# Performance work log

Measured on AMD Instinct MI355X. Metric: run time of the kernel, lower is better.

Reference implementation:

```python
import jax, jax.numpy as jnp
import numpy as np

B, S, D, H = 1, 2048, 768, 12
E, K, I = 8, 2, 1024          # routed experts, top-k, expert inter dim
IS = 2 * I                    # shared-expert inter dim (n_shared_experts * moe_inter_dim)
EPS = 1e-5
ROUTE_SCALE = 1.0


def rmsnorm(x, w, eps=EPS):
    xf = x.astype(jnp.float32)
    return (xf * jax.lax.rsqrt(jnp.mean(xf * xf, axis=-1, keepdims=True) + eps)).astype(x.dtype) * w


def setup_inputs() -> dict:
    key = jax.random.key(0)
    ks = jax.random.split(key, 8)
    sc = 0.02
    return {
        "x": jax.random.normal(ks[0], (B, S, D), jnp.float32),
        "norm1_w": jnp.ones((D,), jnp.float32),
        "norm3_w": jnp.ones((D,), jnp.float32),
        "gate_w": jax.random.normal(ks[1], (E, D), jnp.float32) * sc,
        "w1": jax.random.normal(ks[2], (E, I, D), jnp.float32) * sc,
        "b1": jnp.zeros((E, I), jnp.float32),
        "w2": jax.random.normal(ks[3], (E, D, I), jnp.float32) * sc,
        "b2": jnp.zeros((E, D), jnp.float32),
        "w3": jax.random.normal(ks[4], (E, I, D), jnp.float32) * sc,
        "b3": jnp.zeros((E, I), jnp.float32),
        "fc1_w": jax.random.normal(ks[5], (IS, D), jnp.float32) * sc,
        "fc1_b": jnp.zeros((IS,), jnp.float32),
        "fc2_w": jax.random.normal(ks[6], (D, IS), jnp.float32) * sc,
        "fc2_b": jnp.zeros((D,), jnp.float32),
    }


def _forward(x, norm1_w, norm3_w, gate_w, w1, b1, w2, b2, w3, b3,
             fc1_w, fc1_b, fc2_w, fc2_b):
    b, s, d = x.shape
    hd = d // H

    # ---- self-attention (no qkv/out projections in the original module) ----
    xn = rmsnorm(x, norm1_w)
    qkv = xn.reshape(b, s, H, hd).transpose(0, 2, 1, 3)      # [b,h,s,hd]
    scores = jnp.einsum("bhqd,bhkd->bhqk", qkv, qkv) / np.sqrt(hd)
    attn = jax.nn.softmax(scores, axis=-1)
    ao = jnp.einsum("bhqk,bhkd->bhqd", attn, qkv)
    attn_out = ao.transpose(0, 2, 1, 3).reshape(b, s, d)
    out = x + attn_out

    # ---- MoE on norm3(out) ----
    xf = rmsnorm(out, norm3_w).reshape(-1, d)                # [N, D]
    n = xf.shape[0]

    # Gate: softmax scoring, n_groups=1 (no group masking), no bias (dim != 7168)
    logits = xf @ gate_w.T                                    # [N, E]
    sc = jax.nn.softmax(logits.astype(jnp.float32), axis=-1)  # max-subtract folded in
    _, idx = jax.lax.top_k(sc, K)                             # [N, K]
    weights = jnp.take_along_axis(sc, idx, axis=-1)
    weights = jnp.clip(weights, 1e-7) * ROUTE_SCALE
    weights = weights.astype(xf.dtype)

    # combine matrix: per-token dense expert weights (zeros for unselected)
    cmb = jnp.zeros((n, E), xf.dtype).at[jnp.arange(n)[:, None], idx].add(weights)

    # SwiGLU experts, batched over E (zero combine weight == not dispatched)
    a = jnp.einsum("nd,eid->nei", xf, w1) + b1                # [N,E,I]
    g = jnp.einsum("nd,eid->nei", xf, w3) + b3
    h = jax.nn.silu(a) * g
    eo = jnp.einsum("nei,edi->ned", h, w2) + b2               # [N,E,D]
    y = jnp.einsum("ned,ne->nd", eo, cmb)

    # shared experts (SiLU MLP)
    z = jax.nn.silu(xf @ fc1_w.T + fc1_b) @ fc2_w.T + fc2_b

    moe_out = (y + z).reshape(b, s, d)
    return out + moe_out


def reference(x, norm1_w, norm3_w, gate_w, w1, b1, w2, b2, w3, b3,
              fc1_w, fc1_b, fc2_w, fc2_b):
    return _forward(x, norm1_w, norm3_w, gate_w, w1, b1, w2, b2, w3, b3,
                    fc1_w, fc1_b, fc2_w, fc2_b)
```

## Files before the change

kernel.cpp:

```cpp
#include <hip/hip_runtime.h>
#include <math.h>

#define SEQ    2048
#define DMODEL 768
#define NHEAD  12
#define NEXP   8
#define IDIM   1024
#define ISH    2048
#define KVS    4
#define NE2    10
#define CVT_BLOCKS 10752

typedef unsigned short u16;
typedef short s16x8 __attribute__((ext_vector_type(8)));
typedef u16   u16x8 __attribute__((ext_vector_type(8)));
typedef float f32x4 __attribute__((ext_vector_type(4)));

#define MFMA_BF16(a, b, c) __builtin_amdgcn_mfma_f32_16x16x32_bf16((a), (b), (c), 0, 0, 0)

__device__ __forceinline__ void glds16(const void* g, void* l) {
  __builtin_amdgcn_global_load_lds(
      (const __attribute__((address_space(1))) unsigned int*)g,
      (__attribute__((address_space(3))) unsigned int*)l, 16, 0, 0);
}

__device__ __forceinline__ u16 f2b(float f) {
  unsigned int u = __float_as_uint(f);
  unsigned int r = u + 0x7fffu + ((u >> 16) & 1u);
  return (u16)(r >> 16);
}
__device__ __forceinline__ float b2f(u16 v) {
  return __uint_as_float(((unsigned int)v) << 16);
}

__global__ __launch_bounds__(256) void cvt_all_kernel(
    const float* __restrict__ w1, const float* __restrict__ w3, const float* __restrict__ w2,
    const float* __restrict__ fc1, const float* __restrict__ fc2,
    u16* __restrict__ w1b, u16* __restrict__ w3b, u16* __restrict__ w2b,
    u16* __restrict__ fc1b, u16* __restrict__ fc2b, int* __restrict__ counts,
    const float* __restrict__ x, const float* __restrict__ n1w, u16* __restrict__ xnb) {
  const int tid = threadIdx.x;
  if (blockIdx.x >= CVT_BLOCKS) {
    const int row = blockIdx.x - CVT_BLOCKS;
    const float* r = x + (size_t)row * DMODEL;
    float v0 = r[tid], v1 = r[tid + 256], v2 = r[tid + 512];
    float ss = v0 * v0 + v1 * v1 + v2 * v2;
    __shared__ float red[256];
    red[tid] = ss;
    __syncthreads();
    for (int s = 128; s > 0; s >>= 1) {
      if (tid < s) red[tid] += red[tid + s];
      __syncthreads();
    }
    float rms = rsqrtf(red[0] * (1.f / DMODEL) + 1e-5f);
    u16* ob = xnb + (size_t)row * DMODEL;
    ob[tid]       = f2b(v0 * rms * n1w[tid]);
    ob[tid + 256] = f2b(v1 * rms * n1w[tid + 256]);
    ob[tid + 512] = f2b(v2 * rms * n1w[tid + 512]);
    return;
  }
  if (blockIdx.x == 0 && tid < 16) counts[tid] = 0;
  long i = (long)blockIdx.x * 256 + tid;
  const long NW8 = (long)NEXP * IDIM * DMODEL / 8;
  const long NF8 = (long)ISH * DMODEL / 8;
  const float* s; u16* d; long o;
  if      (i < NW8)             { s = w1;  d = w1b;  o = i; }
  else if (i < 2 * NW8)         { s = w3;  d = w3b;  o = i - NW8; }
  else if (i < 3 * NW8)         { s = w2;  d = w2b;  o = i - 2 * NW8; }
  else if (i < 3 * NW8 + NF8)   { s = fc1; d = fc1b; o = i - 3 * NW8; }
  else if (i < 3 * NW8 + 2*NF8) { s = fc2; d = fc2b; o = i - 3 * NW8 - NF8; }
  else return;
  float4 a = ((const float4*)s)[2 * o], b = ((const float4*)s)[2 * o + 1];
  u16x8 v;
  v[0] = f2b(a.x); v[1] = f2b(a.y); v[2] = f2b(a.z); v[3] = f2b(a.w);
  v[4] = f2b(b.x); v[5] = f2b(b.y); v[6] = f2b(b.z); v[7] = f2b(b.w);
  ((u16x8*)d)[o] = v;
}

__global__ __launch_bounds__(256) void attn_kernel(const u16* __restrict__ xnb,
                                                   u16* __restrict__ Opart,
                                                   float* __restrict__ Mpart,
                                                   float* __restrict__ Lpart) {
  __shared__ u16 Qs[64][72];
  __shared__ u16 Ks[64][72];
  __shared__ u16 Vt[64][72];
  __shared__ u16 Ps[64][72];
  const int h = blockIdx.y, kvs = blockIdx.z;
  const int q0 = blockIdx.x * 64;
  const int tid = threadIdx.x;
  const int lane = tid & 63, w = tid >> 6;
  const int quad = lane >> 4, l15 = lane & 15;
  const size_t hoff = (size_t)h * 64;

  for (int cc = tid; cc < 512; cc += 256) {
    int row = cc >> 3, col8 = (cc & 7) * 8;
    *(u16x8*)&Qs[row][col8] = *(const u16x8*)(xnb + (size_t)(q0 + row) * DMODEL + hoff + col8);
  }
  __syncthreads();
  const s16x8 aq0 = *(const s16x8*)&Qs[16 * w + l15][quad * 8];
  const s16x8 aq1 = *(const s16x8*)&Qs[16 * w + l15][32 + quad * 8];

  f32x4 o[4] = {};
  float mrow[4], lrow[4];
#pragma unroll
  for (int r = 0; r < 4; r++) { mrow[r] = -INFINITY; lrow[r] = 0.f; }

  const int it0 = kvs * (SEQ / 64 / KVS);
  for (int it = 0; it < SEQ / 64 / KVS; it++) {
    const int k0 = (it0 + it) * 64;
    for (int cc = tid; cc < 512; cc += 256) {
      int row = cc >> 3, col8 = (cc & 7) * 8;
      *(u16x8*)&Ks[row][col8] = *(const u16x8*)(xnb + (size_t)(k0 + row) * DMODEL + hoff + col8);
    }
    __syncthreads();

    {
      const int rp = tid & 31, dc = ((tid >> 5) & 7) * 8;
      u16x8 v0 = *(const u16x8*)&Ks[2 * rp][dc];
      u16x8 v1 = *(const u16x8*)&Ks[2 * rp + 1][dc];
#pragma unroll
      for (int j = 0; j < 8; j++) {
        *(unsigned int*)&Vt[dc + j][2 * rp] =
            (unsigned int)v0[j] | ((unsigned int)v1[j] << 16);
      }
    }

    f32x4 s4[4] = {};
#pragma unroll
    for (int jt = 0; jt < 4; jt++) {
      s16x8 b0 = *(const s16x8*)&Ks[16 * jt + l15][quad * 8];
      s16x8 b1 = *(const s16x8*)&Ks[16 * jt + l15][32 + quad * 8];
      s4[jt] = MFMA_BF16(aq0, b0, s4[jt]);
      s4[jt] = MFMA_BF16(aq1, b1, s4[jt]);
      s4[jt] *= 0.125f;
    }

#pragma unroll
    for (int r = 0; r < 4; r++) {
      float mx = mrow[r];
#pragma unroll
      for (int jt = 0; jt < 4; jt++) mx = fmaxf(mx, s4[jt][r]);
#pragma unroll
      for (int m = 1; m <= 8; m <<= 1) mx = fmaxf(mx, __shfl_xor(mx, m, 64));
      float al = __expf(mrow[r] - mx);
      mrow[r] = mx;
      float pv[4], sum = 0.f;
#pragma unroll
      for (int jt = 0; jt < 4; jt++) { pv[jt] = __expf(s4[jt][r] - mx); sum += pv[jt]; }
#pragma unroll
      for (int m = 1; m <= 8; m <<= 1) sum += __shfl_xor(sum, m, 64);
      lrow[r] = lrow[r] * al + sum;
#pragma unroll
      for (int jt = 0; jt < 4; jt++) o[jt][r] *= al;
#pragma unroll
      for (int jt = 0; jt < 4; jt++) Ps[16 * w + quad * 4 + r][16 * jt + l15] = f2b(pv[jt]);
    }
    __syncthreads();

    s16x8 ap0 = *(const s16x8*)&Ps[16 * w + l15][quad * 8];
    s16x8 ap1 = *(const s16x8*)&Ps[16 * w + l15][32 + quad * 8];
#pragma unroll
    for (int jt = 0; jt < 4; jt++) {
      s16x8 bv0 = *(const s16x8*)&Vt[16 * jt + l15][quad * 8];
      s16x8 bv1 = *(const s16x8*)&Vt[16 * jt + l15][32 + quad * 8];
      o[jt] = MFMA_BF16(ap0, bv0, o[jt]);
      o[jt] = MFMA_BF16(ap1, bv1, o[jt]);
    }
  }

  const int hk = h * KVS + kvs;
#pragma unroll
  for (int r = 0; r < 4; r++) {
    int q = q0 + 16 * w + quad * 4 + r;
    size_t base = (size_t)q * (KVS * NHEAD) + hk;
#pragma unroll
    for (int jt = 0; jt < 4; jt++)
      Opart[base * 64 + 16 * jt + l15] = f2b(o[jt][r]);
    if (l15 == 0) {
      Mpart[base] = mrow[r];
      Lpart[base] = lrow[r];
    }
  }
}

__global__ __launch_bounds__(256) void fused_post_kernel(
    const u16* __restrict__ Opart, const float* __restrict__ Mpart,
    const float* __restrict__ Lpart, const float* __restrict__ x,
    const float* __restrict__ n3w, const float* __restrict__ gw,
    u16* __restrict__ xfb, float* __restrict__ out,
    int* __restrict__ counts, int* __restrict__ toklist, float* __restrict__ wtlist) {
  const int tid = threadIdx.x;
  const int lane = tid & 63, w = tid >> 6;
  const int t = blockIdx.x * 4 + w;
  __shared__ float wgtS[4][48];
  __shared__ float LhS[4][12];

  if (lane < 48) {
    float m = Mpart[(size_t)t * 48 + lane];
    float l = Lpart[(size_t)t * 48 + lane];
    float m1 = fmaxf(m, __shfl_xor(m, 1, 64));
    float mh = fmaxf(m1, __shfl_xor(m1, 2, 64));
    float wgt = __expf(m - mh);
    float wl = wgt * l;
    float s1 = wl + __shfl_xor(wl, 1, 64);
    float Lh = s1 + __shfl_xor(s1, 2, 64);
    wgtS[w][lane] = wgt;
    if ((lane & 3) == 0) LhS[w][lane >> 2] = Lh;
  }

  float val[12];
  float ss = 0.f;
  const float* xr = x + (size_t)t * DMODEL;
  float* outr = out + (size_t)t * DMODEL;
#pragma unroll
  for (int ii = 0; ii < 12; ii++) {
    float O = 0.f;
#pragma unroll
    for (int k = 0; k < KVS; k++)
      O += wgtS[w][ii * 4 + k] * b2f(Opart[((size_t)t * 48 + ii * 4 + k) * 64 + lane]);
    float v = xr[ii * 64 + lane] + O / LhS[w][ii];
    outr[ii * 64 + lane] = v;
    val[ii] = v;
    ss += v * v;
  }
#pragma unroll
  for (int off = 32; off >= 1; off >>= 1) ss += __shfl_xor(ss, off, 64);
  float rms = rsqrtf(ss * (1.f / DMODEL) + 1e-5f);

  float ge[NEXP] = {};
#pragma unroll
  for (int ii = 0; ii < 12; ii++) {
    int c = ii * 64 + lane;
    float xn = val[ii] * rms * n3w[c];
    xfb[(size_t)t * DMODEL + c] = f2b(xn);
#pragma unroll
    for (int e = 0; e < NEXP; e++) ge[e] = fmaf(xn, gw[e * DMODEL + c], ge[e]);
  }
#pragma unroll
  for (int off = 32; off >= 1; off >>= 1)
#pragma unroll
    for (int e = 0; e < NEXP; e++) ge[e] += __shfl_xor(ge[e], off, 64);

  if (lane == 0) {
    float p[NEXP], mx = -INFINITY, s = 0.f;
#pragma unroll
    for (int e = 0; e < NEXP; e++) mx = fmaxf(mx, ge[e]);
#pragma unroll
    for (int e = 0; e < NEXP; e++) { p[e] = __expf(ge[e] - mx); s += p[e]; }
    int e0 = 0; float b0 = p[0];
    for (int e = 1; e < NEXP; e++) if (p[e] > b0) { b0 = p[e]; e0 = e; }
    int e1 = -1; float b1v = -1.f;
    for (int e = 0; e < NEXP; e++) if (e != e0 && p[e] > b1v) { b1v = p[e]; e1 = e; }
    float inv = 1.f / s;
    int pos0 = atomicAdd(&counts[e0], 1);
    toklist[e0 * SEQ + pos0] = t;
    wtlist[e0 * SEQ + pos0] = fmaxf(b0 * inv, 1e-7f);
    int pos1 = atomicAdd(&counts[e1], 1);
    toklist[e1 * SEQ + pos1] = t;
    wtlist[e1 * SEQ + pos1] = fmaxf(b1v * inv, 1e-7f);
  }
}

__global__ __launch_bounds__(256) void gemm1_kernel(
    const u16* __restrict__ xfb,
    const u16* __restrict__ w1b, const u16* __restrict__ w3b, const u16* __restrict__ fc1b,
    const float* __restrict__ b1, const float* __restrict__ b3, const float* __restrict__ fc1_b,
    const int* __restrict__ counts, const int* __restrict__ toklist, u16* __restrict__ hb) {
  __shared__ u16 As[64][32];
  __shared__ u16 W1s[128][32];
  __shared__ u16 W3s[128][32];
  __shared__ int rIdx[64];
  const int e = blockIdx.z;
  const bool routed = (e < NEXP);
  int cnt, off;
  if (routed) {
    cnt = counts[e];
    off = 0;
    for (int i = 0; i < e; i++) off += counts[i];
  } else {
    cnt = SEQ;
    off = 2 * SEQ + (e - NEXP) * SEQ;
  }
  const int m0 = blockIdx.y * 64;
  if (m0 >= cnt) return;
  const int n0 = blockIdx.x * 128;
  const int tid = threadIdx.x;
  if (tid < 64) {
    int rr = m0 + tid;
    rIdx[tid] = routed ? toklist[e * SEQ + (rr < cnt ? rr : cnt - 1)] : rr;
  }
  __syncthreads();
  const u16* W1 = routed ? w1b + (size_t)e * IDIM * DMODEL
                         : fc1b + (size_t)(e - NEXP) * IDIM * DMODEL;
  const ptrdiff_t d31 = w3b - w1b;

  const int lane = tid & 63, w = tid >> 6;
  const int quad = lane >> 4, l15 = lane & 15;
  const int wy = w >> 1, wx = w & 1;
  const int srow = lane >> 2;
  const int schunk = ((lane & 3) ^ ((lane >> 3) & 3)) * 8;
  const int cb = (quad ^ ((l15 >> 1) & 3)) * 8;

  const u16* aS   = xfb + (size_t)rIdx[16 * w + srow] * DMODEL + schunk;
  const u16* w1S0 = W1 + (size_t)(n0 + 32 * w + srow) * DMODEL + schunk;
  const u16* w1S1 = W1 + (size_t)(n0 + 32 * w + 16 + srow) * DMODEL + schunk;

  f32x4 acc1[2][4] = {};
  f32x4 acc3[2][4] = {};
  for (int k0 = 0; k0 < DMODEL; k0 += 32) {
    glds16(aS + k0, &As[16 * w][0]);
    glds16(w1S0 + k0, &W1s[32 * w][0]);
    glds16(w1S1 + k0, &W1s[32 * w + 16][0]);
    if (routed) {
      glds16(w1S0 + d31 + k0, &W3s[32 * w][0]);
      glds16(w1S1 + d31 + k0, &W3s[32 * w + 16][0]);
    }
    __syncthreads();
    s16x8 af[2], w1f[4];
#pragma unroll
    for (int i = 0; i < 2; i++) af[i] = *(const s16x8*)&As[32 * wy + 16 * i + l15][cb];
#pragma unroll
    for (int j = 0; j < 4; j++) w1f[j] = *(const s16x8*)&W1s[64 * wx + 16 * j + l15][cb];
#pragma unroll
    for (int i = 0; i < 2; i++)
#pragma unroll
      for (int j = 0; j < 4; j++)
        acc1[i][j] = MFMA_BF16(af[i], w1f[j], acc1[i][j]);
    if (routed) {
      s16x8 w3f[4];
#pragma unroll
      for (int j = 0; j < 4; j++) w3f[j] = *(const s16x8*)&W3s[64 * wx + 16 * j + l15][cb];
#pragma unroll
      for (int i = 0; i < 2; i++)
#pragma unroll
        for (int j = 0; j < 4; j++)
          acc3[i][j] = MFMA_BF16(af[i], w3f[j], acc3[i][j]);
    }
    __syncthreads();
  }

#pragma unroll
  for (int j = 0; j < 4; j++) {
    int n = n0 + 64 * wx + 16 * j + l15;
    float b1v = routed ? b1[e * IDIM + n] : fc1_b[(e - NEXP) * IDIM + n];
    float b3v = routed ? b3[e * IDIM + n] : 0.f;
#pragma unroll
    for (int i = 0; i < 2; i++) {
#pragma unroll
      for (int r = 0; r < 4; r++) {
        int rr = m0 + 32 * wy + 16 * i + quad * 4 + r;
        if (rr < cnt) {
          float a = acc1[i][j][r] + b1v;
          float g = routed ? (acc3[i][j][r] + b3v) : 1.f;
          float hv = a / (1.f + __expf(-a)) * g;
          hb[(size_t)(off + rr) * IDIM + n] = f2b(hv);
        }
      }
    }
  }
}

__global__ __launch_bounds__(256) void gemm2_kernel(
    const u16* __restrict__ hb,
    const u16* __restrict__ w2b, const u16* __restrict__ fc2b,
    const float* __restrict__ b2, const float* __restrict__ fc2_b,
    const int* __restrict__ counts, const int* __restrict__ toklist,
    const float* __restrict__ wtlist, float* __restrict__ out) {
  __shared__ u16 As[64][32];
  __shared__ u16 Ws[128][32];
  const int n0 = blockIdx.x * 128;
  if (n0 >= DMODEL) return;
  const int e = blockIdx.z;
  const bool routed = (e < NEXP);
  int cnt, off;
  if (routed) {
    cnt = counts[e];
    off = 0;
    for (int i = 0; i < e; i++) off += counts[i];
  } else {
    cnt = SEQ;
    off = 2 * SEQ + (e - NEXP) * SEQ;
  }
  const int m0 = blockIdx.y * 64;
  if (m0 >= cnt) return;
  const int tid = threadIdx.x;

  const u16* Wb; int ldw, kof;
  if (routed) { Wb = w2b + (size_t)e * DMODEL * IDIM; ldw = IDIM; kof = 0; }
  else        { Wb = fc2b;                            ldw = ISH;  kof = (e - NEXP) * IDIM; }

  const int lane = tid & 63, w = tid >> 6;
  const int quad = lane >> 4, l15 = lane & 15;
  const int wy = w >> 1, wx = w & 1;
  const int srow = lane >> 2;
  const int schunk = ((lane & 3) ^ ((lane >> 3) & 3)) * 8;
  const int cb = (quad ^ ((l15 >> 1) & 3)) * 8;

  int ra = m0 + 16 * w + srow;
  ra = off + (ra < cnt ? ra : cnt - 1);
  const u16* aS  = hb + (size_t)ra * IDIM + schunk;
  const u16* wS0 = Wb + (size_t)(n0 + 32 * w + srow) * ldw + kof + schunk;
  const u16* wS1 = Wb + (size_t)(n0 + 32 * w + 16 + srow) * ldw + kof + schunk;

  f32x4 acc[2][4] = {};
  for (int k0 = 0; k0 < IDIM; k0 += 32) {
    glds16(aS + k0, &As[16 * w][0]);
    glds16(wS0 + k0, &Ws[32 * w][0]);
    glds16(wS1 + k0, &Ws[32 * w + 16][0]);
    __syncthreads();
    s16x8 af[2], wf[4];
#pragma unroll
    for (int i = 0; i < 2; i++) af[i] = *(const s16x8*)&As[32 * wy + 16 * i + l15][cb];
#pragma unroll
    for (int j = 0; j < 4; j++) wf[j] = *(const s16x8*)&Ws[64 * wx + 16 * j + l15][cb];
#pragma unroll
    for (int i = 0; i < 2; i++)
#pragma unroll
      for (int j = 0; j < 4; j++)
        acc[i][j] = MFMA_BF16(af[i], wf[j], acc[i][j]);
    __syncthreads();
  }

#pragma unroll
  for (int j = 0; j < 4; j++) {
    int n = n0 + 64 * wx + 16 * j + l15;
    float bv = routed ? b2[e * DMODEL + n] : (e == NEXP ? fc2_b[n] : 0.f);
#pragma unroll
    for (int i = 0; i < 2; i++) {
#pragma unroll
      for (int r = 0; r < 4; r++) {
        int rr = m0 + 32 * wy + 16 * i + quad * 4 + r;
        if (rr < cnt) {
          int tok; float wt;
          if (routed) { tok = toklist[e * SEQ + rr]; wt = wtlist[e * SEQ + rr]; }
          else        { tok = rr;                    wt = 1.f; }
          atomicAdd(&out[(size_t)tok * DMODEL + n], wt * (acc[i][j][r] + bv));
        }
      }
    }
  }
}

extern "C" void kernel_launch(void* const* d_in, const int* in_sizes, int n_in,
                              void* d_out, int out_size, void* d_ws, size_t ws_size,
                              hipStream_t stream) {
  const float* x       = (const float*)d_in[0];
  const float* norm1_w = (const float*)d_in[1];
  const float* norm3_w = (const float*)d_in[2];
  const float* gate_w  = (const float*)d_in[3];
  const float* w1      = (const float*)d_in[4];
  const float* b1      = (const float*)d_in[5];
  const float* w2      = (const float*)d_in[6];
  const float* b2      = (const float*)d_in[7];
  const float* w3      = (const float*)d_in[8];
  const float* b3      = (const float*)d_in[9];
  const float* fc1_w   = (const float*)d_in[10];
  const float* fc1_b   = (const float*)d_in[11];
  const float* fc2_w   = (const float*)d_in[12];
  const float* fc2_b   = (const float*)d_in[13];
  float* out = (float*)d_out;

  char* p = (char*)d_ws;
  u16*   xnb    = (u16*)p;   p += (size_t)SEQ * DMODEL * 2;
  u16*   xfb    = (u16*)p;   p += (size_t)SEQ * DMODEL * 2;
  u16*   hb     = (u16*)p;   p += (size_t)4 * SEQ * IDIM * 2;
  u16*   Opart  = (u16*)p;   p += (size_t)KVS * NHEAD * SEQ * 64 * 2;
  float* Mpart  = (float*)p; p += (size_t)KVS * NHEAD * SEQ * 4;
  float* Lpart  = (float*)p; p += (size_t)KVS * NHEAD * SEQ * 4;
  u16*   w1b    = (u16*)p;   p += (size_t)NEXP * IDIM * DMODEL * 2;
  u16*   w3b    = (u16*)p;   p += (size_t)NEXP * IDIM * DMODEL * 2;
  u16*   w2b    = (u16*)p;   p += (size_t)NEXP * DMODEL * IDIM * 2;
  u16*   fc1b   = (u16*)p;   p += (size_t)ISH * DMODEL * 2;
  u16*   fc2b   = (u16*)p;   p += (size_t)DMODEL * ISH * 2;
  int*   counts = (int*)p;   p += 256;
  int*   toklist= (int*)p;   p += (size_t)NEXP * SEQ * 4;
  float* wtlist = (float*)p; p += (size_t)NEXP * SEQ * 4;

  cvt_all_kernel<<<CVT_BLOCKS + SEQ, 256, 0, stream>>>(w1, w3, w2, fc1_w, fc2_w,
                                                       w1b, w3b, w2b, fc1b, fc2b, counts,
                                                       x, norm1_w, xnb);
  attn_kernel<<<dim3(SEQ / 64, NHEAD, KVS), 256, 0, stream>>>(xnb, Opart, Mpart, Lpart);
  fused_post_kernel<<<SEQ / 4, 256, 0, stream>>>(Opart, Mpart, Lpart, x, norm3_w, gate_w,
                                                 xfb, out, counts, toklist, wtlist);
  gemm1_kernel<<<dim3(IDIM / 128, SEQ / 64, NE2), 256, 0, stream>>>(
      xfb, w1b, w3b, fc1b, b1, b3, fc1_b, counts, toklist, hb);
  gemm2_kernel<<<dim3(8, SEQ / 64, NE2), 256, 0, stream>>>(
      hb, w2b, fc2b, b2, fc2_b, counts, toklist, wtlist, out);
  (void)in_sizes; (void)n_in; (void)out_size; (void)ws_size;
}
```

Baseline: 351.0 us.

## Overlap weight conversion with attention, split-K gemm2, one token per post block

The first RMSNorm now runs in its own kernel, and the fp32-to-bf16 weight conversion blocks are merged into the attention launch so the two run concurrently instead of back to back. The post-attention kernel now gives each token a full 256-thread block, stages the partial attention outputs in shared memory, and reduces the sum of squares and gate logits across waves through shared memory. The down-projection GEMM is split four ways along K, which adds more blocks and more atomicAdd traffic to the output; the bias is added only by the first split.

```diff
diff --git a/kernel.cpp b/kernel.cpp
--- a/kernel.cpp
+++ b/kernel.cpp
@@ -9,6 +9,7 @@
 #define ISH    2048
 #define KVS    4
 #define NE2    10
+#define ATTN_BLOCKS 1536
 #define CVT_BLOCKS 10752
 
 typedef unsigned short u16;
@@ -33,61 +34,62 @@
   return __uint_as_float(((unsigned int)v) << 16);
 }
 
-__global__ __launch_bounds__(256) void cvt_all_kernel(
+__global__ __launch_bounds__(256) void rmsnorm_kernel(const float* __restrict__ x,
+                                                      const float* __restrict__ n1w,
+                                                      u16* __restrict__ xnb,
+                                                      int* __restrict__ counts) {
+  const int tid = threadIdx.x;
+  if (blockIdx.x == 0 && tid < 16) counts[tid] = 0;
+  const int row = blockIdx.x;
+  const float* r = x + (size_t)row * DMODEL;
+  float v0 = r[tid], v1 = r[tid + 256], v2 = r[tid + 512];
+  float ss = v0 * v0 + v1 * v1 + v2 * v2;
+  __shared__ float red[256];
+  red[tid] = ss;
+  __syncthreads();
+  for (int s = 128; s > 0; s >>= 1) {
+    if (tid < s) red[tid] += red[tid + s];
+    __syncthreads();
+  }
+  float rms = rsqrtf(red[0] * (1.f / DMODEL) + 1e-5f);
+  u16* ob = xnb + (size_t)row * DMODEL;
+  ob[tid]       = f2b(v0 * rms * n1w[tid]);
+  ob[tid + 256] = f2b(v1 * rms * n1w[tid + 256]);
+  ob[tid + 512] = f2b(v2 * rms * n1w[tid + 512]);
+}
+
+__global__ __launch_bounds__(256) void attn_cvt_kernel(
+    const u16* __restrict__ xnb, u16* __restrict__ Opart,
+    float* __restrict__ Mpart, float* __restrict__ Lpart,
     const float* __restrict__ w1, const float* __restrict__ w3, const float* __restrict__ w2,
     const float* __restrict__ fc1, const float* __restrict__ fc2,
     u16* __restrict__ w1b, u16* __restrict__ w3b, u16* __restrict__ w2b,
-    u16* __restrict__ fc1b, u16* __restrict__ fc2b, int* __restrict__ counts,
-    const float* __restrict__ x, const float* __restrict__ n1w, u16* __restrict__ xnb) {
+    u16* __restrict__ fc1b, u16* __restrict__ fc2b) {
   const int tid = threadIdx.x;
-  if (blockIdx.x >= CVT_BLOCKS) {
-    const int row = blockIdx.x - CVT_BLOCKS;
-    const float* r = x + (size_t)row * DMODEL;
-    float v0 = r[tid], v1 = r[tid + 256], v2 = r[tid + 512];
-    float ss = v0 * v0 + v1 * v1 + v2 * v2;
-    __shared__ float red[256];
-    red[tid] = ss;
-    __syncthreads();
-    for (int s = 128; s > 0; s >>= 1) {
-      if (tid < s) red[tid] += red[tid + s];
-      __syncthreads();
-    }
-    float rms = rsqrtf(red[0] * (1.f / DMODEL) + 1e-5f);
-    u16* ob = xnb + (size_t)row * DMODEL;
-    ob[tid]       = f2b(v0 * rms * n1w[tid]);
-    ob[tid + 256] = f2b(v1 * rms * n1w[tid + 256]);
-    ob[tid + 512] = f2b(v2 * rms * n1w[tid + 512]);
+  if (blockIdx.x >= ATTN_BLOCKS) {
+    long i = (long)(blockIdx.x - ATTN_BLOCKS) * 256 + tid;
+    const long NW8 = (long)NEXP * IDIM * DMODEL / 8;
+    const long NF8 = (long)ISH * DMODEL / 8;
+    const float* s; u16* d; long o;
+    if      (i < NW8)             { s = w1;  d = w1b;  o = i; }
+    else if (i < 2 * NW8)         { s = w3;  d = w3b;  o = i - NW8; }
+    else if (i < 3 * NW8)         { s = w2;  d = w2b;  o = i - 2 * NW8; }
+    else if (i < 3 * NW8 + NF8)   { s = fc1; d = fc1b; o = i - 3 * NW8; }
+    else                          { s = fc2; d = fc2b; o = i - 3 * NW8 - NF8; }
+    float4 a = ((const float4*)s)[2 * o], b = ((const float4*)s)[2 * o + 1];
+    u16x8 v;
+    v[0] = f2b(a.x); v[1] = f2b(a.y); v[2] = f2b(a.z); v[3] = f2b(a.w);
+    v[4] = f2b(b.x); v[5] = f2b(b.y); v[6] = f2b(b.z); v[7] = f2b(b.w);
+    ((u16x8*)d)[o] = v;
     return;
   }
-  if (blockIdx.x == 0 && tid < 16) counts[tid] = 0;
-  long i = (long)blockIdx.x * 256 + tid;
-  const long NW8 = (long)NEXP * IDIM * DMODEL / 8;
-  const long NF8 = (long)ISH * DMODEL / 8;
-  const float* s; u16* d; long o;
-  if      (i < NW8)             { s = w1;  d = w1b;  o = i; }
-  else if (i < 2 * NW8)         { s = w3;  d = w3b;  o = i - NW8; }
-  else if (i < 3 * NW8)         { s = w2;  d = w2b;  o = i - 2 * NW8; }
-  else if (i < 3 * NW8 + NF8)   { s = fc1; d = fc1b; o = i - 3 * NW8; }
-  else if (i < 3 * NW8 + 2*NF8) { s = fc2; d = fc2b; o = i - 3 * NW8 - NF8; }
-  else return;
-  float4 a = ((const float4*)s)[2 * o], b = ((const float4*)s)[2 * o + 1];
-  u16x8 v;
-  v[0] = f2b(a.x); v[1] = f2b(a.y); v[2] = f2b(a.z); v[3] = f2b(a.w);
-  v[4] = f2b(b.x); v[5] = f2b(b.y); v[6] = f2b(b.z); v[7] = f2b(b.w);
-  ((u16x8*)d)[o] = v;
-}
-
-__global__ __launch_bounds__(256) void attn_kernel(const u16* __restrict__ xnb,
-                                                   u16* __restrict__ Opart,
-                                                   float* __restrict__ Mpart,
-                                                   float* __restrict__ Lpart) {
   __shared__ u16 Qs[64][72];
   __shared__ u16 Ks[64][72];
   __shared__ u16 Vt[64][72];
   __shared__ u16 Ps[64][72];
-  const int h = blockIdx.y, kvs = blockIdx.z;
-  const int q0 = blockIdx.x * 64;
-  const int tid = threadIdx.x;
+  const int q0 = (blockIdx.x & 31) * 64;
+  const int h = (blockIdx.x >> 5) % NHEAD;
+  const int kvs = blockIdx.x / (32 * NHEAD);
   const int lane = tid & 63, w = tid >> 6;
   const int quad = lane >> 4, l15 = lane & 15;
   const size_t hoff = (size_t)h * 64;
@@ -189,49 +191,56 @@
     const float* __restrict__ n3w, const float* __restrict__ gw,
     u16* __restrict__ xfb, float* __restrict__ out,
     int* __restrict__ counts, int* __restrict__ toklist, float* __restrict__ wtlist) {
+  const int t = blockIdx.x;
   const int tid = threadIdx.x;
   const int lane = tid & 63, w = tid >> 6;
-  const int t = blockIdx.x * 4 + w;
-  __shared__ float wgtS[4][48];
-  __shared__ float LhS[4][12];
-
-  if (lane < 48) {
-    float m = Mpart[(size_t)t * 48 + lane];
-    float l = Lpart[(size_t)t * 48 + lane];
-    float m1 = fmaxf(m, __shfl_xor(m, 1, 64));
-    float mh = fmaxf(m1, __shfl_xor(m1, 2, 64));
-    float wgt = __expf(m - mh);
-    float wl = wgt * l;
-    float s1 = wl + __shfl_xor(wl, 1, 64);
-    float Lh = s1 + __shfl_xor(s1, 2, 64);
-    wgtS[w][lane] = wgt;
-    if ((lane & 3) == 0) LhS[w][lane >> 2] = Lh;
-  }
-
-  float val[12];
+  __shared__ u16 Os[48 * 64];
+  __shared__ float MsLs[96];
+  __shared__ float ssP[4];
+  __shared__ float geP[4][NEXP];
+
+  const u16* orow = Opart + (size_t)t * (48 * 64);
+  for (int c = tid; c < 384; c += 256)
+    *(u16x8*)&Os[c * 8] = *(const u16x8*)&orow[c * 8];
+  if (tid < 96)
+    MsLs[tid] = (tid < 48) ? Mpart[(size_t)t * 48 + tid]
+                           : Lpart[(size_t)t * 48 + (tid - 48)];
+  __syncthreads();
+
+  float val[3];
   float ss = 0.f;
   const float* xr = x + (size_t)t * DMODEL;
   float* outr = out + (size_t)t * DMODEL;
 #pragma unroll
-  for (int ii = 0; ii < 12; ii++) {
-    float O = 0.f;
-#pragma unroll
-    for (int k = 0; k < KVS; k++)
-      O += wgtS[w][ii * 4 + k] * b2f(Opart[((size_t)t * 48 + ii * 4 + k) * 64 + lane]);
-    float v = xr[ii * 64 + lane] + O / LhS[w][ii];
+  for (int j = 0; j < 3; j++) {
+    const int ii = 3 * w + j;
+    float m0 = MsLs[ii * 4 + 0], m1 = MsLs[ii * 4 + 1];
+    float m2 = MsLs[ii * 4 + 2], m3 = MsLs[ii * 4 + 3];
+    float mh = fmaxf(fmaxf(m0, m1), fmaxf(m2, m3));
+    float c0 = __expf(m0 - mh), c1 = __expf(m1 - mh);
+    float c2 = __expf(m2 - mh), c3 = __expf(m3 - mh);
+    float Lh = c0 * MsLs[48 + ii * 4 + 0] + c1 * MsLs[48 + ii * 4 + 1] +
+               c2 * MsLs[48 + ii * 4 + 2] + c3 * MsLs[48 + ii * 4 + 3];
+    float O = c0 * b2f(Os[(ii * 4 + 0) * 64 + lane]) +
+              c1 * b2f(Os[(ii * 4 + 1) * 64 + lane]) +
+              c2 * b2f(Os[(ii * 4 + 2) * 64 + lane]) +
+              c3 * b2f(Os[(ii * 4 + 3) * 64 + lane]);
+    float v = xr[ii * 64 + lane] + O / Lh;
     outr[ii * 64 + lane] = v;
-    val[ii] = v;
+    val[j] = v;
     ss += v * v;
   }
 #pragma unroll
   for (int off = 32; off >= 1; off >>= 1) ss += __shfl_xor(ss, off, 64);
-  float rms = rsqrtf(ss * (1.f / DMODEL) + 1e-5f);
+  if (lane == 0) ssP[w] = ss;
+  __syncthreads();
+  float rms = rsqrtf((ssP[0] + ssP[1] + ssP[2] + ssP[3]) * (1.f / DMODEL) + 1e-5f);
 
   float ge[NEXP] = {};
 #pragma unroll
-  for (int ii = 0; ii < 12; ii++) {
-    int c = ii * 64 + lane;
-    float xn = val[ii] * rms * n3w[c];
+  for (int j = 0; j < 3; j++) {
+    int c = (3 * w + j) * 64 + lane;
+    float xn = val[j] * rms * n3w[c];
     xfb[(size_t)t * DMODEL + c] = f2b(xn);
 #pragma unroll
     for (int e = 0; e < NEXP; e++) ge[e] = fmaf(xn, gw[e * DMODEL + c], ge[e]);
@@ -240,13 +249,20 @@
   for (int off = 32; off >= 1; off >>= 1)
 #pragma unroll
     for (int e = 0; e < NEXP; e++) ge[e] += __shfl_xor(ge[e], off, 64);
-
-  if (lane == 0) {
+  if (lane == 0)
+#pragma unroll
+    for (int e = 0; e < NEXP; e++) geP[w][e] = ge[e];
+  __syncthreads();
+
+  if (tid == 0) {
     float p[NEXP], mx = -INFINITY, s = 0.f;
 #pragma unroll
-    for (int e = 0; e < NEXP; e++) mx = fmaxf(mx, ge[e]);
-#pragma unroll
-    for (int e = 0; e < NEXP; e++) { p[e] = __expf(ge[e] - mx); s += p[e]; }
+    for (int e = 0; e < NEXP; e++) {
+      p[e] = geP[0][e] + geP[1][e] + geP[2][e] + geP[3][e];
+      mx = fmaxf(mx, p[e]);
+    }
+#pragma unroll
+    for (int e = 0; e < NEXP; e++) { p[e] = __expf(p[e] - mx); s += p[e]; }
     int e0 = 0; float b0 = p[0];
     for (int e = 1; e < NEXP; e++) if (p[e] > b0) { b0 = p[e]; e0 = e; }
     int e1 = -1; float b1v = -1.f;
@@ -370,7 +386,8 @@
   __shared__ u16 Ws[128][32];
   const int n0 = blockIdx.x * 128;
   if (n0 >= DMODEL) return;
-  const int e = blockIdx.z;
+  const int e = blockIdx.z >> 2;
+  const int ks = blockIdx.z & 3;
   const bool routed = (e < NEXP);
   int cnt, off;
   if (routed) {
@@ -388,6 +405,7 @@
   const u16* Wb; int ldw, kof;
   if (routed) { Wb = w2b + (size_t)e * DMODEL * IDIM; ldw = IDIM; kof = 0; }
   else        { Wb = fc2b;                            ldw = ISH;  kof = (e - NEXP) * IDIM; }
+  kof += ks * (IDIM / 4);
 
   const int lane = tid & 63, w = tid >> 6;
   const int quad = lane >> 4, l15 = lane & 15;
@@ -398,12 +416,12 @@
 
   int ra = m0 + 16 * w + srow;
   ra = off + (ra < cnt ? ra : cnt - 1);
-  const u16* aS  = hb + (size_t)ra * IDIM + schunk;
+  const u16* aS  = hb + (size_t)ra * IDIM + ks * (IDIM / 4) + schunk;
   const u16* wS0 = Wb + (size_t)(n0 + 32 * w + srow) * ldw + kof + schunk;
   const u16* wS1 = Wb + (size_t)(n0 + 32 * w + 16 + srow) * ldw + kof + schunk;
 
   f32x4 acc[2][4] = {};
-  for (int k0 = 0; k0 < IDIM; k0 += 32) {
+  for (int k0 = 0; k0 < IDIM / 4; k0 += 32) {
     glds16(aS + k0, &As[16 * w][0]);
     glds16(wS0 + k0, &Ws[32 * w][0]);
     glds16(wS1 + k0, &Ws[32 * w + 16][0]);
@@ -424,7 +442,8 @@
 #pragma unroll
   for (int j = 0; j < 4; j++) {
     int n = n0 + 64 * wx + 16 * j + l15;
-    float bv = routed ? b2[e * DMODEL + n] : (e == NEXP ? fc2_b[n] : 0.f);
+    float bv = 0.f;
+    if (ks == 0) bv = routed ? b2[e * DMODEL + n] : (e == NEXP ? fc2_b[n] : 0.f);
 #pragma unroll
     for (int i = 0; i < 2; i++) {
 #pragma unroll
@@ -476,15 +495,15 @@
   int*   toklist= (int*)p;   p += (size_t)NEXP * SEQ * 4;
   float* wtlist = (float*)p; p += (size_t)NEXP * SEQ * 4;
 
-  cvt_all_kernel<<<CVT_BLOCKS + SEQ, 256, 0, stream>>>(w1, w3, w2, fc1_w, fc2_w,
-                                                       w1b, w3b, w2b, fc1b, fc2b, counts,
-                                                       x, norm1_w, xnb);
-  attn_kernel<<<dim3(SEQ / 64, NHEAD, KVS), 256, 0, stream>>>(xnb, Opart, Mpart, Lpart);
-  fused_post_kernel<<<SEQ / 4, 256, 0, stream>>>(Opart, Mpart, Lpart, x, norm3_w, gate_w,
-                                                 xfb, out, counts, toklist, wtlist);
+  rmsnorm_kernel<<<SEQ, 256, 0, stream>>>(x, norm1_w, xnb, counts);
+  attn_cvt_kernel<<<ATTN_BLOCKS + CVT_BLOCKS, 256, 0, stream>>>(
+      xnb, Opart, Mpart, Lpart, w1, w3, w2, fc1_w, fc2_w,
+      w1b, w3b, w2b, fc1b, fc2b);
+  fused_post_kernel<<<SEQ, 256, 0, stream>>>(Opart, Mpart, Lpart, x, norm3_w, gate_w,
+                                             xfb, out, counts, toklist, wtlist);
   gemm1_kernel<<<dim3(IDIM / 128, SEQ / 64, NE2), 256, 0, stream>>>(
       xfb, w1b, w3b, fc1b, b1, b3, fc1_b, counts, toklist, hb);
-  gemm2_kernel<<<dim3(8, SEQ / 64, NE2), 256, 0, stream>>>(
+  gemm2_kernel<<<dim3(8, SEQ / 64, NE2 * 4), 256, 0, stream>>>(
       hb, w2b, fc2b, b2, fc2_b, counts, toklist, wtlist, out);
   (void)in_sizes; (void)n_in; (void)out_size; (void)ws_size;
 }
```

Measured after the change: 378.8 us. 7.9% more time.
